# Optimization experiments

Hardware: AMD Instinct MI355X
Metric: run time of the kernel (lower is better)

The kernel has to match this reference:

```python
import jax, jax.numpy as jnp
import numpy as np

N = 100000   # nodes
E = 1600000  # edges
D = 128      # in_channels
H = 128      # hidden_dim
L = 3        # num_layers
LH = 128     # lstm_hidden
OUT = 16     # output_dim
G = 128      # graphs in batch
EPS = 1e-5   # BatchNorm eps


def setup_inputs() -> dict:
    key = jax.random.key(0)
    ks = jax.random.split(key, 14)
    x = jax.random.normal(ks[0], (N, D), jnp.float32)
    src = jax.random.randint(ks[1], (E,), 0, N)
    dst = jax.random.randint(ks[2], (E,), 0, N)
    edge_index = jnp.stack([src, dst])
    batch = jnp.sort(jax.random.randint(ks[3], (N,), 0, G))
    Ws = jax.random.normal(ks[4], (L, D, H), jnp.float32) / np.float32(np.sqrt(D))
    bs = jax.random.normal(ks[5], (L, H), jnp.float32) * 0.02
    gammas = 1.0 + 0.1 * jax.random.normal(ks[6], (L, H), jnp.float32)
    betas = 0.1 * jax.random.normal(ks[7], (L, H), jnp.float32)
    rms = 0.1 * jax.random.normal(ks[8], (L, H), jnp.float32)
    rvs = jax.random.uniform(ks[9], (L, H), jnp.float32, 0.5, 1.5)
    W_ih = jax.random.normal(ks[10], (4 * LH, H), jnp.float32) / np.float32(np.sqrt(H))
    W_hh = jax.random.normal(ks[11], (4 * LH, LH), jnp.float32) / np.float32(np.sqrt(LH))
    b_ih = jnp.zeros((4 * LH,), jnp.float32)
    b_hh = jnp.zeros((4 * LH,), jnp.float32)
    W_fc = jax.random.normal(ks[12], (OUT, LH), jnp.float32) / np.float32(np.sqrt(LH))
    b_fc = 0.02 * jax.random.normal(ks[13], (OUT,), jnp.float32)
    return dict(x=x, edge_index=edge_index, batch=batch, Ws=Ws, bs=bs,
                gammas=gammas, betas=betas, rms=rms, rvs=rvs,
                W_ih=W_ih, W_hh=W_hh, b_ih=b_ih, b_hh=b_hh, W_fc=W_fc, b_fc=b_fc)


def reference(x, edge_index, batch, Ws, bs, gammas, betas, rms, rvs,
              W_ih, W_hh, b_ih, b_hh, W_fc, b_fc):
    # GCNConv: add self-loops, symmetric deg^-1/2 normalization
    src, dst = edge_index[0], edge_index[1]
    loop = jnp.arange(N)
    s = jnp.concatenate([src, loop])
    d = jnp.concatenate([dst, loop])
    deg = jax.ops.segment_sum(jnp.ones((E + N,), x.dtype), d, num_segments=N)
    dinv = jax.lax.rsqrt(jnp.maximum(deg, 1.0))  # deg >= 1 due to self-loops
    norm = (dinv[s] * dinv[d])[:, None]          # [E+N, 1]
    h = x
    for l in range(L):
        h = h @ Ws[l]                                                  # [N, H]
        agg = jax.ops.segment_sum(h[s] * norm, d, num_segments=N) + bs[l]
        # BatchNorm (eval: running stats) -> dropout (eval: identity) -> ReLU
        y = (agg - rms[l]) * (gammas[l] * jax.lax.rsqrt(rvs[l] + EPS)) + betas[l]
        h = jax.nn.relu(y)
    # global_mean_pool
    sums = jax.ops.segment_sum(h, batch, num_segments=G)               # [G, H]
    cnt = jax.ops.segment_sum(jnp.ones((N,), h.dtype), batch, num_segments=G)
    pooled = sums / jnp.maximum(cnt, 1.0)[:, None]
    # single-timestep LSTM, h0 = c0 = 0 -> forget gate contributes nothing
    gates = pooled @ W_ih.T + b_ih + b_hh                              # [G, 4*LH]
    i, f, g, o = jnp.split(gates, 4, axis=-1)
    c = jax.nn.sigmoid(i) * jnp.tanh(g)
    hn = jax.nn.sigmoid(o) * jnp.tanh(c)
    return hn @ W_fc.T + b_fc                                          # [G, OUT]
```

## Files before the change

kernel.cpp:

```cpp
#include <hip/hip_runtime.h>
#include <math.h>

constexpr int   NN  = 100000;
constexpr int   EE  = 1600000;
constexpr int   HH  = 128;
constexpr int   GG  = 128;
constexpr float EPSV = 1e-5f;
constexpr int   NSH = 8;
constexpr int   SHN = NN / NSH;
constexpr int   CAP = 210000;
constexpr int   NSB = 32;
constexpr int   SUBW = (SHN + NSB - 1) / NSB;
constexpr int   CAP2 = 8192;
constexpr int   NCH = 64;

typedef __attribute__((ext_vector_type(8))) short  short8;
typedef __attribute__((ext_vector_type(4))) float  f32x4;
typedef __attribute__((ext_vector_type(2))) float  v2f;

__device__ __forceinline__ unsigned short f2bf(float f) {
    union { float f; unsigned u; } v; v.f = f;
    unsigned r = v.u + 0x7FFF + ((v.u >> 16) & 1);
    return (unsigned short)(r >> 16);
}
__device__ __forceinline__ float bf2f(unsigned short b) {
    union { unsigned u; float f; } v; v.u = ((unsigned)b) << 16;
    return v.f;
}

constexpr size_t A256(size_t x) { return (x + 255) & ~(size_t)255; }
constexpr size_t OFF_TL  = 0;
constexpr size_t OFF_DEG = A256(OFF_TL  + (8 + 256) * 4);
constexpr size_t OFF_DNV = A256(OFF_DEG + (size_t)NN * 4);
constexpr size_t OFF_RP  = A256(OFF_DNV + (size_t)NN * 4);
constexpr size_t OFF_SRC = A256(OFF_RP  + (size_t)(NN + 1) * 4);
constexpr size_t OFF_BIN = A256(OFF_SRC + (size_t)EE * 4);
constexpr size_t OFF_BS  = A256(OFF_BIN + (size_t)8 * CAP * 4);
constexpr size_t OFF_XB  = A256(OFF_BS  + 512 * 4);
constexpr size_t OFF_B2  = OFF_XB;
constexpr size_t OFF_HW  = A256(OFF_XB  + (size_t)NN * HH * 2);
constexpr size_t OFF_H0  = A256(OFF_HW  + (size_t)NN * HH * 2);
constexpr size_t OFF_PL  = A256(OFF_H0  + (size_t)NN * HH * 2);

__global__ __launch_bounds__(256) void k_bin(const int* __restrict__ src,
                                             const int* __restrict__ dst,
                                             unsigned* __restrict__ bins,
                                             unsigned* __restrict__ gtail) {
    __shared__ unsigned sbin[8][1024];
    __shared__ unsigned scnt[8];
    __shared__ unsigned sbase[8];
    int t = threadIdx.x;
    if (t < 8) scnt[t] = 0;
    __syncthreads();
    int i = blockIdx.x * 256 + t;
    const int nvec = EE / 4;
    if (i < nvec) {
        int4 d = ((const int4*)dst)[i];
        int4 s = ((const int4*)src)[i];
        int dd[4] = {d.x, d.y, d.z, d.w};
        int ss[4] = {s.x, s.y, s.z, s.w};
#pragma unroll
        for (int c = 0; c < 4; ++c) {
            int sh = dd[c] / SHN;
            unsigned p = atomicAdd(&scnt[sh], 1u);
            sbin[sh][p] = ((unsigned)(dd[c] - sh * SHN) << 17) | (unsigned)ss[c];
        }
    }
    __syncthreads();
    if (t < 8) sbase[t] = atomicAdd(&gtail[t], scnt[t]);
    __syncthreads();
    for (int s = 0; s < 8; ++s) {
        unsigned cnt = scnt[s], base = sbase[s];
        if (base >= (unsigned)CAP) continue;
        if (base + cnt > (unsigned)CAP) cnt = CAP - base;
        for (unsigned j = t; j < cnt; j += 256)
            bins[(size_t)s * CAP + base + j] = sbin[s][j];
    }
}

__global__ __launch_bounds__(256) void k_bin2(const unsigned* __restrict__ bins,
                                              const unsigned* __restrict__ gtail,
                                              unsigned* __restrict__ bins2,
                                              unsigned* __restrict__ tail2) {
    __shared__ unsigned staged[(CAP + NCH - 1) / NCH + 64];
    __shared__ unsigned cnt[NSB], base[NSB], cur[NSB], gbase[NSB];
    int t = threadIdx.x;
    int shard = blockIdx.x >> 6, chunk = blockIdx.x & 63;
    unsigned m = gtail[shard];
    if (m > (unsigned)CAP) m = CAP;
    unsigned csz = (m + NCH - 1) / NCH;
    unsigned i0 = chunk * csz;
    unsigned i1 = i0 + csz; if (i1 > m) i1 = m;
    if (i0 >= m) return;
    const unsigned* bb = bins + (size_t)shard * CAP;

    if (t < NSB) cnt[t] = 0;
    __syncthreads();
    for (unsigned i = i0 + t; i < i1; i += 256)
        atomicAdd(&cnt[(bb[i] >> 17) / SUBW], 1u);
    __syncthreads();
    if (t == 0) {
        unsigned run = 0;
        for (int sb = 0; sb < NSB; ++sb) { base[sb] = run; run += cnt[sb]; }
    }
    __syncthreads();
    if (t < NSB) {
        gbase[t] = atomicAdd(&tail2[shard * NSB + t], cnt[t]);
        cur[t] = base[t];
    }
    __syncthreads();
    for (unsigned i = i0 + t; i < i1; i += 256) {
        unsigned u = bb[i];
        unsigned dl = u >> 17;
        unsigned sb = dl / SUBW;
        unsigned p = atomicAdd(&cur[sb], 1u);
        staged[p] = ((dl - sb * SUBW) << 17) | (u & 0x1FFFFu);
    }
    __syncthreads();
    int wv = t >> 6, ln = t & 63;
    for (int sb = wv; sb < NSB; sb += 4) {
        unsigned c = cnt[sb], gb = gbase[sb], lb = base[sb];
        if (gb >= (unsigned)CAP2) continue;
        if (gb + c > (unsigned)CAP2) c = CAP2 - gb;
        unsigned* dstp = bins2 + (size_t)(shard * NSB + sb) * CAP2 + gb;
        for (unsigned j = ln; j < c; j += 64) dstp[j] = staged[lb + j];
    }
}

__global__ __launch_bounds__(256) void k_hist2(const unsigned* __restrict__ bins2,
                                               const unsigned* __restrict__ tail2,
                                               int* __restrict__ deg) {
    int b = blockIdx.x;
    int shard = b >> 5, sb = b & 31;
    int lo = sb * SUBW;
    int hi = lo + SUBW; if (hi > SHN) hi = SHN;
    int nn = hi - lo;
    __shared__ int hist[SUBW];
    int t = threadIdx.x;
    for (int i = t; i < nn; i += 256) hist[i] = 0;
    __syncthreads();
    unsigned m = tail2[b];
    if (m > (unsigned)CAP2) m = CAP2;
    const unsigned* bb = bins2 + (size_t)b * CAP2;
    unsigned nv = m >> 2;
    for (unsigned i = t; i < nv; i += 256) {
        uint4 u = ((const uint4*)bb)[i];
        atomicAdd(&hist[u.x >> 17], 1);
        atomicAdd(&hist[u.y >> 17], 1);
        atomicAdd(&hist[u.z >> 17], 1);
        atomicAdd(&hist[u.w >> 17], 1);
    }
    for (unsigned i = (m & ~3u) + t; i < m; i += 256)
        atomicAdd(&hist[bb[i] >> 17], 1);
    __syncthreads();
    int gbase = shard * SHN + lo;
    for (int i = t; i < nn; i += 256) deg[gbase + i] = hist[i];
}

__global__ __launch_bounds__(1024) void k_scan_local(const int* __restrict__ deg,
                                                     int* __restrict__ row_ptr,
                                                     int* __restrict__ bsum) {
    __shared__ int s[1024];
    int t = threadIdx.x;
    int i = blockIdx.x * 1024 + t;
    int v = (i < NN) ? deg[i] : 0;
    s[t] = v;
    __syncthreads();
    for (int off = 1; off < 1024; off <<= 1) {
        int u = (t >= off) ? s[t - off] : 0;
        __syncthreads();
        s[t] += u;
        __syncthreads();
    }
    if (i < NN) row_ptr[i] = s[t] - v;
    if (t == 1023) bsum[blockIdx.x] = s[1023];
}

__global__ void k_scan_blocks(int* __restrict__ bsum, int nb) {
    __shared__ int s[128];
    int t = threadIdx.x;
    int v = (t < nb) ? bsum[t] : 0;
    s[t] = v;
    __syncthreads();
    for (int off = 1; off < 128; off <<= 1) {
        int u = (t >= off) ? s[t - off] : 0;
        __syncthreads();
        s[t] += u;
        __syncthreads();
    }
    if (t < nb) bsum[t] = s[t] - v;
}

__global__ void k_scan_add(int* __restrict__ row_ptr, const int* __restrict__ bsum,
                           const int* __restrict__ deg, float* __restrict__ dinv) {
    int i = blockIdx.x * 256 + threadIdx.x;
    if (i < NN) {
        row_ptr[i] += bsum[i >> 10];
        dinv[i] = rsqrtf((float)(deg[i] + 1));
    }
    if (i == 0) row_ptr[NN] = EE;
}

__global__ __launch_bounds__(256) void k_scatter4(const unsigned* __restrict__ bins2,
                                                  const unsigned* __restrict__ tail2,
                                                  const int* __restrict__ rp,
                                                  int* __restrict__ ssrc) {
    int b = blockIdx.x;
    int shard = b >> 5, sb = b & 31;
    int lo = sb * SUBW;
    int hi = lo + SUBW; if (hi > SHN) hi = SHN;
    int nn = hi - lo;
    int gbase = shard * SHN + lo;
    __shared__ int cur[SUBW];
    int t = threadIdx.x;
    for (int i = t; i < nn; i += 256) cur[i] = rp[gbase + i];
    __syncthreads();
    unsigned m = tail2[b];
    if (m > (unsigned)CAP2) m = CAP2;
    const unsigned* bb = bins2 + (size_t)b * CAP2;
    unsigned nv = m >> 2;
    for (unsigned i = t; i < nv; i += 256) {
        uint4 u = ((const uint4*)bb)[i];
        int p;
        p = atomicAdd(&cur[u.x >> 17], 1); ssrc[p] = (int)(u.x & 0x1FFFFu);
        p = atomicAdd(&cur[u.y >> 17], 1); ssrc[p] = (int)(u.y & 0x1FFFFu);
        p = atomicAdd(&cur[u.z >> 17], 1); ssrc[p] = (int)(u.z & 0x1FFFFu);
        p = atomicAdd(&cur[u.w >> 17], 1); ssrc[p] = (int)(u.w & 0x1FFFFu);
    }
    for (unsigned i = (m & ~3u) + t; i < m; i += 256) {
        unsigned u = bb[i];
        int p = atomicAdd(&cur[u >> 17], 1);
        ssrc[p] = (int)(u & 0x1FFFFu);
    }
}

__global__ void k_cvt(const float* __restrict__ x, unsigned short* __restrict__ xb) {
    int i = blockIdx.x * 256 + threadIdx.x;
    if (i < NN * (HH / 4)) {
        float4 v = ((const float4*)x)[i];
        ushort4 o;
        o.x = f2bf(v.x); o.y = f2bf(v.y); o.z = f2bf(v.z); o.w = f2bf(v.w);
        ((ushort4*)xb)[i] = o;
    }
}

__global__ __launch_bounds__(256) void gemm_mfma(const unsigned short* __restrict__ A,
                                                 const float* __restrict__ W,
                                                 unsigned short* __restrict__ C, int nrows) {
    __shared__ unsigned short smem[2 * 64 * 136];
    unsigned short* WtH = smem;
    unsigned short* WtL = smem + 64 * 136;

    int t = threadIdx.x;
    int row0 = blockIdx.x * 128;
    int c0   = blockIdx.y * 64;

    for (int idx = t; idx < 64 * 128; idx += 256) {
        int k = idx >> 6, c = idx & 63;
        float w = W[k * 128 + c0 + c];
        unsigned short hb = f2bf(w);
        unsigned short lb = f2bf(w - bf2f(hb));
        WtH[c * 136 + k] = hb;
        WtL[c * 136 + k] = lb;
    }
    __syncthreads();

    int wv = t >> 6, lane = t & 63, m = lane & 15, q = lane >> 4;
    long rowA = row0 + wv * 32 + m;
    long rowB = rowA + 16;

    f32x4 acc[2][4] = {};
    for (int kc = 0; kc < 4; ++kc) {
        int ko = kc * 32 + q * 8;
        short8 a0 = {}, a1 = {};
        if (rowA < nrows) a0 = *(const short8*)(A + rowA * 128 + ko);
        if (rowB < nrows) a1 = *(const short8*)(A + rowB * 128 + ko);
#pragma unroll
        for (int ct = 0; ct < 4; ++ct) {
            short8 bh = *(const short8*)(WtH + (ct * 16 + m) * 136 + ko);
            short8 bl = *(const short8*)(WtL + (ct * 16 + m) * 136 + ko);
            acc[0][ct] = __builtin_amdgcn_mfma_f32_16x16x32_bf16(a0, bh, acc[0][ct], 0, 0, 0);
            acc[0][ct] = __builtin_amdgcn_mfma_f32_16x16x32_bf16(a0, bl, acc[0][ct], 0, 0, 0);
            acc[1][ct] = __builtin_amdgcn_mfma_f32_16x16x32_bf16(a1, bh, acc[1][ct], 0, 0, 0);
            acc[1][ct] = __builtin_amdgcn_mfma_f32_16x16x32_bf16(a1, bl, acc[1][ct], 0, 0, 0);
        }
    }

    __syncthreads();
    unsigned short* Cs = smem;
#pragma unroll
    for (int rt = 0; rt < 2; ++rt)
#pragma unroll
        for (int ct = 0; ct < 4; ++ct)
#pragma unroll
            for (int r = 0; r < 4; ++r) {
                int rl = wv * 32 + rt * 16 + q * 4 + r;
                Cs[rl * 68 + ct * 16 + m] = f2bf(acc[rt][ct][r]);
            }
    __syncthreads();
    for (int idx = t; idx < 128 * 16; idx += 256) {
        int row = idx >> 4, ch = idx & 15;
        long grow = row0 + row;
        if (grow < nrows)
            *(ushort4*)(C + grow * 128 + c0 + ch * 4) = *(const ushort4*)(Cs + row * 68 + ch * 4);
    }
}

__global__ __launch_bounds__(256) void k_agg(const unsigned short* __restrict__ hw,
                                             const int* __restrict__ rp,
                                             const int* __restrict__ ssrc,
                                             const float* __restrict__ dinv,
                                             const float* __restrict__ bsl,
                                             const float* __restrict__ gamma,
                                             const float* __restrict__ beta,
                                             const float* __restrict__ rm,
                                             const float* __restrict__ rv,
                                             unsigned short* __restrict__ out) {
    int lane = threadIdx.x & 63;
    int c2   = lane * 2;
    int n = blockIdx.x * 4 + (threadIdx.x >> 6);
    if (n >= NN) return;
    int beg = rp[n], end = rp[n + 1];

    v2f acc0 = {0.f, 0.f}, acc1 = {0.f, 0.f};

    for (int chunk = beg; chunk < end; chunk += 64) {
        int l = chunk + lane;
        bool valid = (l < end);
        int   e  = valid ? ssrc[l] : n;
        float dv = valid ? dinv[e] : 0.f;
        int cnt = end - chunk;
        if (cnt > 64) cnt = 64;
        for (int jb = 0; jb < cnt; jb += 8) {
#pragma unroll
            for (int j = 0; j < 8; ++j) {
                int s    = __builtin_amdgcn_readlane(e, jb + j);
                float ds = __int_as_float(
                               __builtin_amdgcn_readlane(__float_as_int(dv), jb + j));
                unsigned u = *(const unsigned*)(hw + (size_t)s * HH + c2);
                v2f vv;
                vv.x = __int_as_float((int)(u << 16));
                vv.y = __int_as_float((int)(u & 0xffff0000u));
                v2f d2 = {ds, ds};
                if (j & 1) acc1 += d2 * vv;
                else       acc0 += d2 * vv;
            }
        }
    }
    v2f a = acc0 + acc1;

    float di = dinv[n];
    {
        unsigned u = *(const unsigned*)(hw + (size_t)n * HH + c2);
        v2f vv;
        vv.x = __int_as_float((int)(u << 16));
        vv.y = __int_as_float((int)(u & 0xffff0000u));
        v2f d2 = {di, di};
        a += d2 * vv;
    }
    a.x *= di;
    a.y *= di;

    float g0 = gamma[c2],   g1 = gamma[c2 + 1];
    float r0 = rv[c2],      r1 = rv[c2 + 1];
    float s0 = g0 * rsqrtf(r0 + EPSV);
    float s1 = g1 * rsqrtf(r1 + EPSV);
    float b0 = fmaf(bsl[c2]     - rm[c2],     s0, beta[c2]);
    float b1 = fmaf(bsl[c2 + 1] - rm[c2 + 1], s1, beta[c2 + 1]);
    float y0 = fmaxf(fmaf(a.x, s0, b0), 0.f);
    float y1 = fmaxf(fmaf(a.y, s1, b1), 0.f);
    ushort2 o;
    o.x = f2bf(y0);
    o.y = f2bf(y1);
    *(ushort2*)(out + (size_t)n * HH + c2) = o;
}

__global__ __launch_bounds__(128) void k_pool(const unsigned short* __restrict__ h,
                                              const int* __restrict__ batch,
                                              float* __restrict__ pooled,
                                              float* __restrict__ cnt) {
    int t = threadIdx.x;
    const int chunk = (NN + 1023) / 1024;
    int n0 = blockIdx.x * chunk;
    if (n0 >= NN) return;
    int n1 = n0 + chunk;
    if (n1 > NN) n1 = NN;
    int cur = batch[n0];
    float acc = 0.f;
    int k = 0;
    for (int n = n0; n < n1; ++n) {
        int b = batch[n];
        if (b != cur) {
            atomicAdd(&pooled[(size_t)cur * 128 + t], acc);
            if (t == 0) atomicAdd(&cnt[cur], (float)k);
            acc = 0.f; k = 0; cur = b;
        }
        acc += bf2f(h[(size_t)n * 128 + t]);
        ++k;
    }
    atomicAdd(&pooled[(size_t)cur * 128 + t], acc);
    if (t == 0) atomicAdd(&cnt[cur], (float)k);
}

__global__ __launch_bounds__(128) void k_head(const float* __restrict__ pooled,
                                              const float* __restrict__ cnt,
                                              const float* __restrict__ W_ih,
                                              const float* __restrict__ b_ih,
                                              const float* __restrict__ b_hh,
                                              const float* __restrict__ W_fc,
                                              const float* __restrict__ b_fc,
                                              float* __restrict__ out) {
    __shared__ float pm[128];
    __shared__ float gate[512];
    __shared__ float hn[128];
    int g = blockIdx.x, t = threadIdx.x;
    float cdiv = fmaxf(cnt[g], 1.0f);
    pm[t] = pooled[(size_t)g * 128 + t] / cdiv;
    __syncthreads();
    for (int j = t; j < 512; j += 128) {
        float acc = b_ih[j] + b_hh[j];
        const float* w = W_ih + (size_t)j * 128;
#pragma unroll 8
        for (int k = 0; k < 128; ++k) acc = fmaf(pm[k], w[k], acc);
        gate[j] = acc;
    }
    __syncthreads();
    {
        float gi = gate[t], gg = gate[256 + t], go = gate[384 + t];
        float cc = (1.f / (1.f + expf(-gi))) * tanhf(gg);
        hn[t] = (1.f / (1.f + expf(-go))) * tanhf(cc);
    }
    __syncthreads();
    if (t < 16) {
        float acc = b_fc[t];
        const float* w = W_fc + (size_t)t * 128;
#pragma unroll 8
        for (int k = 0; k < 128; ++k) acc = fmaf(hn[k], w[k], acc);
        out[(size_t)g * 16 + t] = acc;
    }
}

extern "C" void kernel_launch(void* const* d_in, const int* in_sizes, int n_in,
                              void* d_out, int out_size, void* d_ws, size_t ws_size,
                              hipStream_t stream) {
    const float* x      = (const float*)d_in[0];
    const int*   ei     = (const int*)d_in[1];
    const int*   src    = ei;
    const int*   dst    = ei + EE;
    const int*   batch  = (const int*)d_in[2];
    const float* Ws     = (const float*)d_in[3];
    const float* bs     = (const float*)d_in[4];
    const float* gammas = (const float*)d_in[5];
    const float* betas  = (const float*)d_in[6];
    const float* rms    = (const float*)d_in[7];
    const float* rvs    = (const float*)d_in[8];
    const float* W_ih   = (const float*)d_in[9];
    const float* b_ih   = (const float*)d_in[11];
    const float* b_hh   = (const float*)d_in[12];
    const float* W_fc   = (const float*)d_in[13];
    const float* b_fc   = (const float*)d_in[14];
    float* out = (float*)d_out;

    char* w = (char*)d_ws;
    unsigned*       gtail  = (unsigned*)(w + OFF_TL);
    unsigned*       tail2  = gtail + 8;
    int*            deg    = (int*)(w + OFF_DEG);
    float*          dinv   = (float*)(w + OFF_DNV);
    int*            rp     = (int*)(w + OFF_RP);
    int*            ssrc   = (int*)(w + OFF_SRC);
    unsigned*       bins   = (unsigned*)(w + OFF_BIN);
    unsigned*       bins2  = (unsigned*)(w + OFF_B2);
    int*            bsum   = (int*)(w + OFF_BS);
    unsigned short* xb     = (unsigned short*)(w + OFF_XB);
    unsigned short* hwb    = (unsigned short*)(w + OFF_HW);
    unsigned short* h0     = (unsigned short*)(w + OFF_H0);
    float*          pooled = (float*)(w + OFF_PL);
    float*          cntb   = pooled + (size_t)GG * HH;

    hipMemsetAsync(gtail, 0, (8 + 256) * 4, stream);
    hipMemsetAsync(pooled, 0, ((size_t)GG * HH + GG) * 4, stream);

    k_bin<<<(EE / 4 + 255) / 256, 256, 0, stream>>>(src, dst, bins, gtail);
    k_bin2<<<NSH * NCH, 256, 0, stream>>>(bins, gtail, bins2, tail2);
    k_hist2<<<256, 256, 0, stream>>>(bins2, tail2, deg);
    const int nscan = (NN + 1023) / 1024;
    k_scan_local<<<nscan, 1024, 0, stream>>>(deg, rp, bsum);
    k_scan_blocks<<<1, 128, 0, stream>>>(bsum, nscan);
    k_scan_add<<<(NN + 255) / 256, 256, 0, stream>>>(rp, bsum, deg, dinv);
    k_scatter4<<<256, 256, 0, stream>>>(bins2, tail2, rp, ssrc);
    k_cvt<<<(NN * 32 + 255) / 256, 256, 0, stream>>>(x, xb);

    const unsigned short* hin = xb;
    dim3 ggrid((NN + 127) / 128, 2);
    for (int l = 0; l < 3; ++l) {
        gemm_mfma<<<ggrid, 256, 0, stream>>>(hin, Ws + (size_t)l * 128 * 128, hwb, NN);
        k_agg<<<(NN + 3) / 4, 256, 0, stream>>>(hwb, rp, ssrc, dinv,
                                                bs + l * 128, gammas + l * 128, betas + l * 128,
                                                rms + l * 128, rvs + l * 128, h0);
        hin = h0;
    }
    k_pool<<<1024, 128, 0, stream>>>(h0, batch, pooled, cntb);
    k_head<<<GG, 128, 0, stream>>>(pooled, cntb, W_ih, b_ih, b_hh, W_fc, b_fc, out);
}
```

Baseline: 489.0 us.

## Fuse degree histogram with row-pointer scan, fold fp32 conversion into first GEMM

The separate deg write plus three-kernel global scan is replaced by a single-block scan over the 256 sub-bin tails, followed by a per-bin local prefix scan inside the histogram kernel that writes row_ptr and dinv directly. The pooled-buffer memset moves into that tail-scan kernel. The x-to-bf16 conversion kernel is removed; layer 0's GEMM reads fp32 x and converts in registers. Each GEMM block now loads its A rows once and computes both 64-column halves, instead of using a 2-wide grid that loads A twice. This cuts kernel launches and global traffic, at the cost of more register pressure and serialised W staging within a block.

```diff
diff --git a/kernel.cpp b/kernel.cpp
--- a/kernel.cpp
+++ b/kernel.cpp
@@ -30,15 +30,12 @@
 
 constexpr size_t A256(size_t x) { return (x + 255) & ~(size_t)255; }
 constexpr size_t OFF_TL  = 0;
-constexpr size_t OFF_DEG = A256(OFF_TL  + (8 + 256) * 4);
-constexpr size_t OFF_DNV = A256(OFF_DEG + (size_t)NN * 4);
+constexpr size_t OFF_DNV = A256(OFF_TL  + (8 + 256 + 256) * 4);
 constexpr size_t OFF_RP  = A256(OFF_DNV + (size_t)NN * 4);
 constexpr size_t OFF_SRC = A256(OFF_RP  + (size_t)(NN + 1) * 4);
 constexpr size_t OFF_BIN = A256(OFF_SRC + (size_t)EE * 4);
-constexpr size_t OFF_BS  = A256(OFF_BIN + (size_t)8 * CAP * 4);
-constexpr size_t OFF_XB  = A256(OFF_BS  + 512 * 4);
-constexpr size_t OFF_B2  = OFF_XB;
-constexpr size_t OFF_HW  = A256(OFF_XB  + (size_t)NN * HH * 2);
+constexpr size_t OFF_B2  = A256(OFF_BIN + (size_t)8 * CAP * 4);
+constexpr size_t OFF_HW  = A256(OFF_B2  + (size_t)256 * CAP2 * 4);
 constexpr size_t OFF_H0  = A256(OFF_HW  + (size_t)NN * HH * 2);
 constexpr size_t OFF_PL  = A256(OFF_H0  + (size_t)NN * HH * 2);
 
@@ -127,15 +124,37 @@
     }
 }
 
-__global__ __launch_bounds__(256) void k_hist2(const unsigned* __restrict__ bins2,
+__global__ __launch_bounds__(256) void k_tailscan(const unsigned* __restrict__ tail2,
+                                                  unsigned* __restrict__ sbase,
+                                                  float* __restrict__ pooled) {
+    __shared__ unsigned sa[256], sd[256];
+    int t = threadIdx.x;
+    unsigned v = tail2[t];
+    sa[t] = v;
+    __syncthreads();
+    unsigned* s = sa; unsigned* d = sd;
+    for (int off = 1; off < 256; off <<= 1) {
+        d[t] = s[t] + ((t >= off) ? s[t - off] : 0u);
+        __syncthreads();
+        unsigned* tmp = s; s = d; d = tmp;
+    }
+    sbase[t] = s[t] - v;
+    for (int i = t; i < GG * HH + GG; i += 256) pooled[i] = 0.f;
+}
+
+__global__ __launch_bounds__(256) void k_hist3(const unsigned* __restrict__ bins2,
                                                const unsigned* __restrict__ tail2,
-                                               int* __restrict__ deg) {
+                                               const unsigned* __restrict__ sbase,
+                                               int* __restrict__ rp,
+                                               float* __restrict__ dinv) {
     int b = blockIdx.x;
     int shard = b >> 5, sb = b & 31;
     int lo = sb * SUBW;
     int hi = lo + SUBW; if (hi > SHN) hi = SHN;
     int nn = hi - lo;
+    int gbase = shard * SHN + lo;
     __shared__ int hist[SUBW];
+    __shared__ int sa[512], sd[512];
     int t = threadIdx.x;
     for (int i = t; i < nn; i += 256) hist[i] = 0;
     __syncthreads();
@@ -153,52 +172,22 @@
     for (unsigned i = (m & ~3u) + t; i < m; i += 256)
         atomicAdd(&hist[bb[i] >> 17], 1);
     __syncthreads();
-    int gbase = shard * SHN + lo;
-    for (int i = t; i < nn; i += 256) deg[gbase + i] = hist[i];
-}
-
-__global__ __launch_bounds__(1024) void k_scan_local(const int* __restrict__ deg,
-                                                     int* __restrict__ row_ptr,
-                                                     int* __restrict__ bsum) {
-    __shared__ int s[1024];
-    int t = threadIdx.x;
-    int i = blockIdx.x * 1024 + t;
-    int v = (i < NN) ? deg[i] : 0;
-    s[t] = v;
-    __syncthreads();
-    for (int off = 1; off < 1024; off <<= 1) {
-        int u = (t >= off) ? s[t - off] : 0;
+    sa[t]       = (t < nn)       ? hist[t]       : 0;
+    sa[t + 256] = (t + 256 < nn) ? hist[t + 256] : 0;
+    __syncthreads();
+    int* s = sa; int* d = sd;
+    for (int off = 1; off < 512; off <<= 1) {
+        d[t]       = s[t]       + ((t >= off)       ? s[t - off]       : 0);
+        d[t + 256] = s[t + 256] + ((t + 256 >= off) ? s[t + 256 - off] : 0);
         __syncthreads();
-        s[t] += u;
-        __syncthreads();
-    }
-    if (i < NN) row_ptr[i] = s[t] - v;
-    if (t == 1023) bsum[blockIdx.x] = s[1023];
-}
-
-__global__ void k_scan_blocks(int* __restrict__ bsum, int nb) {
-    __shared__ int s[128];
-    int t = threadIdx.x;
-    int v = (t < nb) ? bsum[t] : 0;
-    s[t] = v;
-    __syncthreads();
-    for (int off = 1; off < 128; off <<= 1) {
-        int u = (t >= off) ? s[t - off] : 0;
-        __syncthreads();
-        s[t] += u;
-        __syncthreads();
-    }
-    if (t < nb) bsum[t] = s[t] - v;
-}
-
-__global__ void k_scan_add(int* __restrict__ row_ptr, const int* __restrict__ bsum,
-                           const int* __restrict__ deg, float* __restrict__ dinv) {
-    int i = blockIdx.x * 256 + threadIdx.x;
-    if (i < NN) {
-        row_ptr[i] += bsum[i >> 10];
-        dinv[i] = rsqrtf((float)(deg[i] + 1));
-    }
-    if (i == 0) row_ptr[NN] = EE;
+        int* tmp = s; s = d; d = tmp;
+    }
+    unsigned base = sbase[b];
+    for (int i = t; i < nn; i += 256) {
+        rp[gbase + i]   = (int)(base + (i ? (unsigned)s[i - 1] : 0u));
+        dinv[gbase + i] = rsqrtf((float)(hist[i] + 1));
+    }
+    if (b == 255 && t == 0) rp[NN] = EE;
 }
 
 __global__ __launch_bounds__(256) void k_scatter4(const unsigned* __restrict__ bins2,
@@ -234,75 +223,90 @@
     }
 }
 
-__global__ void k_cvt(const float* __restrict__ x, unsigned short* __restrict__ xb) {
-    int i = blockIdx.x * 256 + threadIdx.x;
-    if (i < NN * (HH / 4)) {
-        float4 v = ((const float4*)x)[i];
-        ushort4 o;
-        o.x = f2bf(v.x); o.y = f2bf(v.y); o.z = f2bf(v.z); o.w = f2bf(v.w);
-        ((ushort4*)xb)[i] = o;
-    }
-}
-
-__global__ __launch_bounds__(256) void gemm_mfma(const unsigned short* __restrict__ A,
+template<bool FP32A>
+__global__ __launch_bounds__(256) void gemm_mfma(const void* __restrict__ Ap,
                                                  const float* __restrict__ W,
                                                  unsigned short* __restrict__ C, int nrows) {
-    __shared__ unsigned short smem[2 * 64 * 136];
-    unsigned short* WtH = smem;
-    unsigned short* WtL = smem + 64 * 136;
-
+    __shared__ unsigned short WtH[64 * 136];
+    __shared__ unsigned short WtL[64 * 136];
     int t = threadIdx.x;
     int row0 = blockIdx.x * 128;
-    int c0   = blockIdx.y * 64;
-
-    for (int idx = t; idx < 64 * 128; idx += 256) {
-        int k = idx >> 6, c = idx & 63;
-        float w = W[k * 128 + c0 + c];
-        unsigned short hb = f2bf(w);
-        unsigned short lb = f2bf(w - bf2f(hb));
-        WtH[c * 136 + k] = hb;
-        WtL[c * 136 + k] = lb;
-    }
-    __syncthreads();
-
     int wv = t >> 6, lane = t & 63, m = lane & 15, q = lane >> 4;
     long rowA = row0 + wv * 32 + m;
     long rowB = rowA + 16;
 
-    f32x4 acc[2][4] = {};
+    short8 a[2][4];
+#pragma unroll
     for (int kc = 0; kc < 4; ++kc) {
         int ko = kc * 32 + q * 8;
-        short8 a0 = {}, a1 = {};
-        if (rowA < nrows) a0 = *(const short8*)(A + rowA * 128 + ko);
-        if (rowB < nrows) a1 = *(const short8*)(A + rowB * 128 + ko);
-#pragma unroll
-        for (int ct = 0; ct < 4; ++ct) {
-            short8 bh = *(const short8*)(WtH + (ct * 16 + m) * 136 + ko);
-            short8 bl = *(const short8*)(WtL + (ct * 16 + m) * 136 + ko);
-            acc[0][ct] = __builtin_amdgcn_mfma_f32_16x16x32_bf16(a0, bh, acc[0][ct], 0, 0, 0);
-            acc[0][ct] = __builtin_amdgcn_mfma_f32_16x16x32_bf16(a0, bl, acc[0][ct], 0, 0, 0);
-            acc[1][ct] = __builtin_amdgcn_mfma_f32_16x16x32_bf16(a1, bh, acc[1][ct], 0, 0, 0);
-            acc[1][ct] = __builtin_amdgcn_mfma_f32_16x16x32_bf16(a1, bl, acc[1][ct], 0, 0, 0);
-        }
-    }
-
-    __syncthreads();
-    unsigned short* Cs = smem;
-#pragma unroll
-    for (int rt = 0; rt < 2; ++rt)
-#pragma unroll
-        for (int ct = 0; ct < 4; ++ct)
-#pragma unroll
-            for (int r = 0; r < 4; ++r) {
-                int rl = wv * 32 + rt * 16 + q * 4 + r;
-                Cs[rl * 68 + ct * 16 + m] = f2bf(acc[rt][ct][r]);
+        if (FP32A) {
+            const float* Af = (const float*)Ap;
+            float4 f0 = {0,0,0,0}, f1 = {0,0,0,0}, g0 = {0,0,0,0}, g1 = {0,0,0,0};
+            if (rowA < nrows) {
+                f0 = *(const float4*)(Af + rowA * 128 + ko);
+                f1 = *(const float4*)(Af + rowA * 128 + ko + 4);
             }
-    __syncthreads();
-    for (int idx = t; idx < 128 * 16; idx += 256) {
-        int row = idx >> 4, ch = idx & 15;
-        long grow = row0 + row;
-        if (grow < nrows)
-            *(ushort4*)(C + grow * 128 + c0 + ch * 4) = *(const ushort4*)(Cs + row * 68 + ch * 4);
+            if (rowB < nrows) {
+                g0 = *(const float4*)(Af + rowB * 128 + ko);
+                g1 = *(const float4*)(Af + rowB * 128 + ko + 4);
+            }
+            union { short8 s; unsigned short u[8]; } ua, ub;
+            ua.u[0] = f2bf(f0.x); ua.u[1] = f2bf(f0.y); ua.u[2] = f2bf(f0.z); ua.u[3] = f2bf(f0.w);
+            ua.u[4] = f2bf(f1.x); ua.u[5] = f2bf(f1.y); ua.u[6] = f2bf(f1.z); ua.u[7] = f2bf(f1.w);
+            ub.u[0] = f2bf(g0.x); ub.u[1] = f2bf(g0.y); ub.u[2] = f2bf(g0.z); ub.u[3] = f2bf(g0.w);
+            ub.u[4] = f2bf(g1.x); ub.u[5] = f2bf(g1.y); ub.u[6] = f2bf(g1.z); ub.u[7] = f2bf(g1.w);
+            a[0][kc] = ua.s; a[1][kc] = ub.s;
+        } else {
+            const unsigned short* Ab = (const unsigned short*)Ap;
+            short8 z = {};
+            a[0][kc] = (rowA < nrows) ? *(const short8*)(Ab + rowA * 128 + ko) : z;
+            a[1][kc] = (rowB < nrows) ? *(const short8*)(Ab + rowB * 128 + ko) : z;
+        }
+    }
+
+    for (int half = 0; half < 2; ++half) {
+        int c0 = half * 64;
+        __syncthreads();
+        for (int idx = t; idx < 64 * 128; idx += 256) {
+            int k = idx >> 6, c = idx & 63;
+            float w = W[k * 128 + c0 + c];
+            unsigned short hb = f2bf(w);
+            WtH[c * 136 + k] = hb;
+            WtL[c * 136 + k] = f2bf(w - bf2f(hb));
+        }
+        __syncthreads();
+        f32x4 acc[2][4] = {};
+#pragma unroll
+        for (int kc = 0; kc < 4; ++kc) {
+            int ko = kc * 32 + q * 8;
+#pragma unroll
+            for (int ct = 0; ct < 4; ++ct) {
+                short8 bh = *(const short8*)(WtH + (ct * 16 + m) * 136 + ko);
+                short8 bl = *(const short8*)(WtL + (ct * 16 + m) * 136 + ko);
+                acc[0][ct] = __builtin_amdgcn_mfma_f32_16x16x32_bf16(a[0][kc], bh, acc[0][ct], 0, 0, 0);
+                acc[0][ct] = __builtin_amdgcn_mfma_f32_16x16x32_bf16(a[0][kc], bl, acc[0][ct], 0, 0, 0);
+                acc[1][ct] = __builtin_amdgcn_mfma_f32_16x16x32_bf16(a[1][kc], bh, acc[1][ct], 0, 0, 0);
+                acc[1][ct] = __builtin_amdgcn_mfma_f32_16x16x32_bf16(a[1][kc], bl, acc[1][ct], 0, 0, 0);
+            }
+        }
+        __syncthreads();
+        unsigned short* Cs = WtH;
+#pragma unroll
+        for (int rt = 0; rt < 2; ++rt)
+#pragma unroll
+            for (int ct = 0; ct < 4; ++ct)
+#pragma unroll
+                for (int r = 0; r < 4; ++r) {
+                    int rl = wv * 32 + rt * 16 + q * 4 + r;
+                    Cs[rl * 68 + ct * 16 + m] = f2bf(acc[rt][ct][r]);
+                }
+        __syncthreads();
+        for (int idx = t; idx < 128 * 16; idx += 256) {
+            int row = idx >> 4, ch = idx & 15;
+            long grow = row0 + row;
+            if (grow < nrows)
+                *(ushort4*)(C + grow * 128 + c0 + ch * 4) = *(const ushort4*)(Cs + row * 68 + ch * 4);
+        }
     }
 }
 
@@ -464,40 +468,34 @@
     char* w = (char*)d_ws;
     unsigned*       gtail  = (unsigned*)(w + OFF_TL);
     unsigned*       tail2  = gtail + 8;
-    int*            deg    = (int*)(w + OFF_DEG);
+    unsigned*       sbase  = gtail + 8 + 256;
     float*          dinv   = (float*)(w + OFF_DNV);
     int*            rp     = (int*)(w + OFF_RP);
     int*            ssrc   = (int*)(w + OFF_SRC);
     unsigned*       bins   = (unsigned*)(w + OFF_BIN);
     unsigned*       bins2  = (unsigned*)(w + OFF_B2);
-    int*            bsum   = (int*)(w + OFF_BS);
-    unsigned short* xb     = (unsigned short*)(w + OFF_XB);
     unsigned short* hwb    = (unsigned short*)(w + OFF_HW);
     unsigned short* h0     = (unsigned short*)(w + OFF_H0);
     float*          pooled = (float*)(w + OFF_PL);
     float*          cntb   = pooled + (size_t)GG * HH;
 
     hipMemsetAsync(gtail, 0, (8 + 256) * 4, stream);
-    hipMemsetAsync(pooled, 0, ((size_t)GG * HH + GG) * 4, stream);
 
     k_bin<<<(EE / 4 + 255) / 256, 256, 0, stream>>>(src, dst, bins, gtail);
     k_bin2<<<NSH * NCH, 256, 0, stream>>>(bins, gtail, bins2, tail2);
-    k_hist2<<<256, 256, 0, stream>>>(bins2, tail2, deg);
-    const int nscan = (NN + 1023) / 1024;
-    k_scan_local<<<nscan, 1024, 0, stream>>>(deg, rp, bsum);
-    k_scan_blocks<<<1, 128, 0, stream>>>(bsum, nscan);
-    k_scan_add<<<(NN + 255) / 256, 256, 0, stream>>>(rp, bsum, deg, dinv);
+    k_tailscan<<<1, 256, 0, stream>>>(tail2, sbase, pooled);
+    k_hist3<<<256, 256, 0, stream>>>(bins2, tail2, sbase, rp, dinv);
     k_scatter4<<<256, 256, 0, stream>>>(bins2, tail2, rp, ssrc);
-    k_cvt<<<(NN * 32 + 255) / 256, 256, 0, stream>>>(x, xb);
-
-    const unsigned short* hin = xb;
-    dim3 ggrid((NN + 127) / 128, 2);
+
+    dim3 ggrid((NN + 127) / 128);
     for (int l = 0; l < 3; ++l) {
-        gemm_mfma<<<ggrid, 256, 0, stream>>>(hin, Ws + (size_t)l * 128 * 128, hwb, NN);
+        if (l == 0)
+            gemm_mfma<true><<<ggrid, 256, 0, stream>>>(x, Ws, hwb, NN);
+        else
+            gemm_mfma<false><<<ggrid, 256, 0, stream>>>(h0, Ws + (size_t)l * 128 * 128, hwb, NN);
         k_agg<<<(NN + 3) / 4, 256, 0, stream>>>(hwb, rp, ssrc, dinv,
                                                 bs + l * 128, gammas + l * 128, betas + l * 128,
                                                 rms + l * 128, rvs + l * 128, h0);
-        hin = h0;
     }
     k_pool<<<1024, 128, 0, stream>>>(h0, batch, pooled, cntb);
     k_head<<<GG, 128, 0, stream>>>(pooled, cntb, W_ih, b_ih, b_hh, W_fc, b_fc, out);
```

Measured after the change: 475.5 us. 2.8% less time.
